# Kernel tuning notes

Measured on AMD Instinct MI355X. Metric: run time of the kernel, lower is better.

The kernel has to match this reference:

```python
import jax, jax.numpy as jnp
import numpy as np

EPS = 1e-5
elu = jax.nn.elu

def bn(x, g, b):
    # BatchNorm (training-mode stats), channel axis = 1
    axes = tuple(i for i in range(x.ndim) if i != 1)
    m = x.mean(axes, keepdims=True)
    v = x.var(axes, keepdims=True)
    shp = [1] * x.ndim; shp[1] = -1
    return g.reshape(shp) * (x - m) * jax.lax.rsqrt(v + EPS) + b.reshape(shp)

def setup_inputs() -> dict:
    key = jax.random.key(0)
    B, N, M, K, C, H, O = 8, 8192, 2048, 16, 128, 64, 256
    ks = jax.random.split(key, 16)
    d = {}
    d['q_points'] = jax.random.normal(ks[0], (B, 3, M), jnp.float32)
    d['s_points'] = jax.random.normal(ks[1], (B, 3, N), jnp.float32)
    d['s_feats'] = jax.random.normal(ks[2], (B, C, N), jnp.float32)
    d['f1_w'] = jax.random.normal(ks[3], (H, 3), jnp.float32) * 0.1
    d['f1_b'] = jnp.zeros((H,), jnp.float32); d['f1_g'] = jnp.ones((H,), jnp.float32); d['f1_be'] = jnp.zeros((H,), jnp.float32)
    d['f2_w'] = jax.random.normal(ks[4], (H, H), jnp.float32) * 0.1
    d['f2_b'] = jnp.zeros((H,), jnp.float32); d['f2_g'] = jnp.ones((H,), jnp.float32); d['f2_be'] = jnp.zeros((H,), jnp.float32)
    d['stem_w'] = jax.random.normal(ks[5], (K * K, 3, K), jnp.float32) * 0.1
    d['stem_b'] = jnp.zeros((K * K,), jnp.float32); d['stem_g'] = jnp.ones((K * K,), jnp.float32); d['stem_be'] = jnp.zeros((K * K,), jnp.float32)
    d['x1_w'] = jax.random.normal(ks[6], (K, K, K), jnp.float32) * 0.1
    d['x1_b'] = jnp.zeros((K * K,), jnp.float32); d['x1_g'] = jnp.ones((K * K,), jnp.float32); d['x1_be'] = jnp.zeros((K * K,), jnp.float32)
    d['x2_w'] = jax.random.normal(ks[7], (K, K, K), jnp.float32) * 0.1
    d['x2_b'] = jnp.zeros((K * K,), jnp.float32); d['x2_g'] = jnp.ones((K * K,), jnp.float32); d['x2_be'] = jnp.zeros((K * K,), jnp.float32)
    d['dw_w'] = jax.random.normal(ks[8], (C + H, K), jnp.float32) * 0.1
    d['pw_w'] = jax.random.normal(ks[9], (O, C + H), jnp.float32) * 0.1
    d['pw_b'] = jnp.zeros((O,), jnp.float32); d['sep_g'] = jnp.ones((O,), jnp.float32); d['sep_be'] = jnp.zeros((O,), jnp.float32)
    d['neighbor_indices'] = jax.random.randint(ks[10], (B, M, K), 0, N, jnp.int64)
    return d

def reference(q_points, s_points, s_feats, f1_w, f1_b, f1_g, f1_be,
              f2_w, f2_b, f2_g, f2_be, stem_w, stem_b, stem_g, stem_be,
              x1_w, x1_b, x1_g, x1_be, x2_w, x2_b, x2_g, x2_be,
              dw_w, pw_w, pw_b, sep_g, sep_be, neighbor_indices):
    B, _, M = q_points.shape
    K = neighbor_indices.shape[2]
    bidx = jnp.arange(B)[:, None, None]
    # group_gather: [B,3,M,K] neighbor coords, centered on queries
    sp = jnp.swapaxes(s_points, 1, 2)                      # [B,N,3]
    aligned = jnp.transpose(sp[bidx, neighbor_indices], (0, 3, 1, 2)) - q_points[:, :, :, None]
    sf = jnp.swapaxes(s_feats, 1, 2)                       # [B,N,C]
    nbr = jnp.transpose(sf[bidx, neighbor_indices], (0, 3, 1, 2))  # [B,C,M,K]
    # f_shared_mlp: two 1x1 conv blocks (conv -> ELU -> BN)
    h = bn(elu(jnp.einsum('bcmk,oc->bomk', aligned, f1_w) + f1_b[None, :, None, None]), f1_g, f1_be)
    h = bn(elu(jnp.einsum('bcmk,oc->bomk', h, f2_w) + f2_b[None, :, None, None]), f2_g, f2_be)
    nf = jnp.concatenate([nbr, h], axis=1)                 # [B,C+H,M,K]
    # X-transform shared MLP: stem Conv2d(3 -> K*K, (1,K))
    t = jnp.einsum('bcmk,ock->bom', aligned, stem_w) + stem_b[None, :, None]
    t = bn(elu(t), stem_g, stem_be).reshape(B, K, K, M)    # [B,g,j,M]
    for w, bb, g, be in ((x1_w, x1_b, x1_g, x1_be), (x2_w, x2_b, x2_g, x2_be)):
        # grouped Conv2d(K -> K*K, (K,1), groups=K)
        y = jnp.einsum('bgjm,gpj->bgpm', t, w) + bb.reshape(1, K, K, 1)
        y = bn(elu(y.reshape(B, K * K, M)), g, be).reshape(B, K, K, M)
        t = jnp.swapaxes(y, 1, 2)                          # XReshape transpose(1,2)
    x = jnp.transpose(t, (0, 3, 2, 1))                     # [B,M,K,K]
    # batched matmul: feats^T @ X
    qf = jnp.einsum('bcmk,bmkl->bcml', nf, x)              # [B,C+H,M,K]
    # SeparableConv2d (1,K): depthwise over K then pointwise 1x1, ELU, BN
    dw = jnp.einsum('bcmk,ck->bcm', qf, dw_w)
    out = jnp.einsum('bcm,oc->bom', dw, pw_w) + pw_b[None, :, None]
    out = bn(elu(out), sep_g, sep_be)                      # [B,O,M]
    return out
```

## Files before the change

### kernel.cpp

```cpp
#include <hip/hip_runtime.h>
#include <hip/hip_bf16.h>
#include <cstddef>
#include <cstdint>

constexpr int cB = 8, cN = 8192, cM = 2048, cK = 16, cC = 128, cH = 64, cO = 256, cCH = 192;
constexpr int NPTS = cB * cM;
constexpr float cEPS = 1e-5f;

typedef __attribute__((ext_vector_type(8))) short short8;
typedef __attribute__((ext_vector_type(4))) float f32x4;

constexpr size_t ACC_BN1 = 0, ACC_BN2 = 128, ACC_STEM = 256, ACC_X1 = 768, ACC_X2 = 1280, ACC_FIN = 1792;
constexpr size_t OFF_SFT = 8192;
constexpr size_t OFF_H1  = OFF_SFT + (size_t)cB * cN * 64;
constexpr size_t OFF_TST = OFF_H1 + (size_t)NPTS * 512;
constexpr size_t OFF_Y1  = OFF_TST + (size_t)NPTS * 128;
constexpr size_t OFF_Y2  = OFF_Y1 + (size_t)NPTS * 256;
constexpr size_t OFF_DW  = OFF_Y1;
constexpr size_t WS_FLOATS = OFF_Y2 + (size_t)NPTS * 256;

__device__ __forceinline__ float eluf(float x) { return x > 0.f ? x : __expf(x) - 1.f; }

__device__ __forceinline__ uint32_t pk2bf(float a, float b) {
    uint32_t ua = __float_as_uint(a); ua += 0x7FFFu + ((ua >> 16) & 1u);
    uint32_t ub = __float_as_uint(b); ub += 0x7FFFu + ((ub >> 16) & 1u);
    return (ua >> 16) | (ub & 0xFFFF0000u);
}
__device__ __forceinline__ float bf_lo(uint32_t u) { return __uint_as_float(u << 16); }
__device__ __forceinline__ float bf_hi(uint32_t u) { return __uint_as_float(u & 0xFFFF0000u); }
__device__ __forceinline__ uint16_t f2bf_u(float a) {
    uint32_t ua = __float_as_uint(a); ua += 0x7FFFu + ((ua >> 16) & 1u);
    return (uint16_t)(ua >> 16);
}

#define WAVE_SYNC() do { asm volatile("s_waitcnt lgkmcnt(0)" ::: "memory"); \
                         __builtin_amdgcn_sched_barrier(0); } while (0)

__global__ __launch_bounds__(256) void k_tr(const float* __restrict__ sf, float* __restrict__ ws) {
    __shared__ float tA[32][33];
    __shared__ float tBt[32][33];
    int b = blockIdx.z, n0 = blockIdx.x * 32, c0 = blockIdx.y * 32;
    int tx = threadIdx.x, ty = threadIdx.y;
    #pragma unroll
    for (int j = 0; j < 32; j += 8) {
        tA[ty + j][tx]  = sf[((size_t)b * cC + (c0 + ty + j)) * cN + n0 + tx];
        tBt[ty + j][tx] = sf[((size_t)b * cC + 64 + (c0 + ty + j)) * cN + n0 + tx];
    }
    __syncthreads();
    uint32_t* out = (uint32_t*)(ws + OFF_SFT);
    #pragma unroll
    for (int j = 0; j < 32; j += 8)
        out[((size_t)b * cN + (n0 + ty + j)) * 64 + c0 + tx] = pk2bf(tA[tx][ty + j], tBt[tx][ty + j]);
}

__global__ __launch_bounds__(256) void kA(const float* __restrict__ qp, const float* __restrict__ sp,
        const float* __restrict__ f1w, const float* __restrict__ f1b,
        const float* __restrict__ stw, const float* __restrict__ stb,
        const int* __restrict__ nidx, float* __restrict__ ws) {
    __shared__ float alw[4][4][48];
    __shared__ __align__(16) uint16_t albs[16][64];
    __shared__ __align__(16) uint16_t bounce[4][16][64];
    __shared__ float red[640];
    int t = threadIdx.x, lane = t & 63, w = t >> 6;
    int ncol = lane & 15, g = lane >> 4;
    for (int l = t; l < 640; l += 256) red[l] = 0.f;
    __syncthreads();
    short8 bfr[4][2];
    float sbias[4];
    #pragma unroll
    for (int tt = 0; tt < 4; tt++) {
        int o = w*64 + tt*16 + ncol;
        sbias[tt] = stb[o];
        #pragma unroll
        for (int s = 0; s < 2; s++) {
            short8 bb;
            #pragma unroll
            for (int j = 0; j < 8; j++) {
                int Kk = s*32 + g*8 + j;
                bb[j] = (Kk < 48) ? (short)f2bf_u(stw[(size_t)o*48 + Kk]) : (short)0;
            }
            bfr[tt][s] = bb;
        }
    }
    float w0 = f1w[lane*3], w1 = f1w[lane*3+1], w2 = f1w[lane*3+2], fb = f1b[lane];
    int pt0 = blockIdx.x * 16;
    {
        int p = lane >> 4, k = lane & 15;
        int row = w*4 + p;
        int pt = pt0 + row, b = pt >> 11, m = pt & (cM - 1);
        int id = nidx[(size_t)pt * cK + k];
        #pragma unroll
        for (int c = 0; c < 3; c++) {
            float v = sp[((size_t)b*3 + c)*cN + id] - qp[((size_t)b*3 + c)*cM + m];
            alw[w][p][c*16 + k] = v;
            int bo = ((c*16 + k)*2) ^ ((row & 7) << 4);
            *(uint16_t*)((char*)&albs[row][0] + bo) = f2bf_u(v);
        }
        int bo = ((48 + k)*2) ^ ((row & 7) << 4);
        *(uint16_t*)((char*)&albs[row][0] + bo) = 0;
    }
    WAVE_SYNC();
    uint4* h1q4 = (uint4*)(ws + OFF_H1);
    float ps1 = 0, pss1 = 0;
    for (int p = 0; p < 4; p++) {
        int pt = pt0 + w*4 + p;
        #pragma unroll
        for (int k = 0; k < 16; k++) {
            float a0 = alw[w][p][k], a1 = alw[w][p][16 + k], a2 = alw[w][p][32 + k];
            float e = eluf(fb + w0*a0 + w1*a1 + w2*a2);
            ps1 += e; pss1 += e*e;
            bounce[w][k][lane] = f2bf_u(e);
        }
        WAVE_SYNC();
        const uint4* src = (const uint4*)&bounce[w][0][0];
        h1q4[(size_t)pt*128 + lane]      = src[lane];
        h1q4[(size_t)pt*128 + 64 + lane] = src[64 + lane];
        WAVE_SYNC();
    }
    atomicAdd(&red[512 + lane], ps1); atomicAdd(&red[576 + lane], pss1);
    __syncthreads();
    uint16_t* tstt = (uint16_t*)&bounce[0][0][0];
    short8 a0, a1;
    {
        int b0 = (g*16) ^ ((ncol & 7) << 4);
        int b1 = (64 + g*16) ^ ((ncol & 7) << 4);
        a0 = *(const short8*)((const char*)&albs[ncol][0] + b0);
        a1 = *(const short8*)((const char*)&albs[ncol][0] + b1);
    }
    #pragma unroll
    for (int tt = 0; tt < 4; tt++) {
        f32x4 acc = {0.f, 0.f, 0.f, 0.f};
        acc = __builtin_amdgcn_mfma_f32_16x16x32_bf16(a0, bfr[tt][0], acc, 0, 0, 0);
        acc = __builtin_amdgcn_mfma_f32_16x16x32_bf16(a1, bfr[tt][1], acc, 0, 0, 0);
        int o = w*64 + tt*16 + ncol;
        float ps2 = 0, pss2 = 0;
        #pragma unroll
        for (int r = 0; r < 4; r++) {
            float e = eluf(acc[r] + sbias[tt]);
            ps2 += e; pss2 += e*e;
            tstt[(g*4 + r)*256 + o] = f2bf_u(e);
        }
        atomicAdd(&red[o], ps2); atomicAdd(&red[256 + o], pss2);
    }
    __syncthreads();
    {
        uint4* tst4 = (uint4*)(ws + OFF_TST);
        const uint4* srcT = (const uint4*)tstt;
        tst4[(size_t)pt0*32 + t]       = srcT[t];
        tst4[(size_t)pt0*32 + 256 + t] = srcT[256 + t];
    }
    atomicAdd(&ws[ACC_STEM + t], red[t]);
    atomicAdd(&ws[ACC_STEM + 256 + t], red[256 + t]);
    if (t < 64) { atomicAdd(&ws[ACC_BN1 + t], red[512 + t]); atomicAdd(&ws[ACC_BN1 + 64 + t], red[576 + t]); }
}

__global__ __launch_bounds__(256) void kE(const float* __restrict__ x1w, const float* __restrict__ x1b,
        const float* __restrict__ stg, const float* __restrict__ stbe, float* __restrict__ ws) {
    __shared__ float xw[256 * 17];
    __shared__ float ts[4][4][256];
    __shared__ float red[512];
    int t = threadIdx.x, lane = t & 63, w = t >> 6;
    for (int l = t; l < 4096; l += 256) xw[(l >> 4)*17 + (l & 15)] = x1w[l];
    for (int l = t; l < 512; l += 256) red[l] = 0.f;
    float sscl[4], sshf[4];
    #pragma unroll
    for (int i = 0; i < 4; i++) {
        int ch = lane*4 + i;
        float mn = ws[ACC_STEM + ch] * (1.f/16384.f);
        float vr = ws[ACC_STEM + 256 + ch] * (1.f/16384.f) - mn*mn;
        float s = stg[ch] * rsqrtf(vr + cEPS);
        sscl[i] = s; sshf[i] = stbe[ch] - mn*s;
    }
    float xb[4];
    #pragma unroll
    for (int q = 0; q < 4; q++) xb[q] = x1b[lane + 64*q];
    __syncthreads();
    const uint16_t* tstb = (const uint16_t*)(ws + OFF_TST);
    int pt0 = blockIdx.x * 16 + w * 4;
    #pragma unroll
    for (int p = 0; p < 4; p++) {
        uint2 v2 = *(const uint2*)&tstb[(size_t)(pt0 + p)*256 + lane*4];
        ts[w][p][lane*4+0] = sscl[0]*bf_lo(v2.x) + sshf[0];
        ts[w][p][lane*4+1] = sscl[1]*bf_hi(v2.x) + sshf[1];
        ts[w][p][lane*4+2] = sscl[2]*bf_lo(v2.y) + sshf[2];
        ts[w][p][lane*4+3] = sscl[3]*bf_hi(v2.y) + sshf[3];
    }
    WAVE_SYNC();
    float ps[4] = {0,0,0,0}, pss[4] = {0,0,0,0};
    #pragma unroll
    for (int q = 0; q < 4; q++) {
        int o = lane + 64*q, g = o >> 4;
        float accp[4] = {xb[q], xb[q], xb[q], xb[q]};
        #pragma unroll
        for (int j4 = 0; j4 < 4; j4++) {
            float s0 = xw[o*17 + j4*4], s1 = xw[o*17 + j4*4+1], s2 = xw[o*17 + j4*4+2], s3 = xw[o*17 + j4*4+3];
            #pragma unroll
            for (int p = 0; p < 4; p++) {
                float4 a = *(const float4*)&ts[w][p][g*16 + j4*4];
                accp[p] += s0*a.x + s1*a.y + s2*a.z + s3*a.w;
            }
        }
        #pragma unroll
        for (int p = 0; p < 4; p++) {
            float e = eluf(accp[p]);
            ps[q] += e; pss[q] += e*e;
            ws[OFF_Y1 + (size_t)(pt0 + p)*256 + o] = e;
        }
    }
    #pragma unroll
    for (int q = 0; q < 4; q++) {
        atomicAdd(&red[lane + 64*q], ps[q]);
        atomicAdd(&red[256 + lane + 64*q], pss[q]);
    }
    __syncthreads();
    atomicAdd(&ws[ACC_X1 + t], red[t]); atomicAdd(&ws[ACC_X1 + 256 + t], red[256 + t]);
}

__global__ __launch_bounds__(256) void kG(const float* __restrict__ x2w, const float* __restrict__ x2b,
        const float* __restrict__ x1g, const float* __restrict__ x1be, float* __restrict__ ws) {
    __shared__ float xw[256 * 17];
    __shared__ float ts[4][4][256];
    __shared__ float red[512];
    int t = threadIdx.x, lane = t & 63, w = t >> 6;
    for (int l = t; l < 4096; l += 256) xw[(l >> 4)*17 + (l & 15)] = x2w[l];
    for (int l = t; l < 512; l += 256) red[l] = 0.f;
    float sscl[4], sshf[4];
    #pragma unroll
    for (int i = 0; i < 4; i++) {
        int ch = lane*4 + i;
        float mn = ws[ACC_X1 + ch] * (1.f/16384.f);
        float vr = ws[ACC_X1 + 256 + ch] * (1.f/16384.f) - mn*mn;
        float s = x1g[ch] * rsqrtf(vr + cEPS);
        sscl[i] = s; sshf[i] = x1be[ch] - mn*s;
    }
    float xb[4];
    #pragma unroll
    for (int q = 0; q < 4; q++) xb[q] = x2b[lane + 64*q];
    __syncthreads();
    int pt0 = blockIdx.x * 16 + w * 4;
    #pragma unroll
    for (int p = 0; p < 4; p++) {
        float4 v = *(const float4*)&ws[OFF_Y1 + (size_t)(pt0 + p)*256 + lane*4];
        float vv[4] = { sscl[0]*v.x + sshf[0], sscl[1]*v.y + sshf[1],
                        sscl[2]*v.z + sshf[2], sscl[3]*v.w + sshf[3] };
        #pragma unroll
        for (int i = 0; i < 4; i++) {
            int ch = lane*4 + i;
            ts[w][p][((ch & 15) << 4) | (ch >> 4)] = vv[i];
        }
    }
    WAVE_SYNC();
    float ps[4] = {0,0,0,0}, pss[4] = {0,0,0,0};
    #pragma unroll
    for (int q = 0; q < 4; q++) {
        int o = lane + 64*q, g = o >> 4;
        float accp[4] = {xb[q], xb[q], xb[q], xb[q]};
        #pragma unroll
        for (int j4 = 0; j4 < 4; j4++) {
            float s0 = xw[o*17 + j4*4], s1 = xw[o*17 + j4*4+1], s2 = xw[o*17 + j4*4+2], s3 = xw[o*17 + j4*4+3];
            #pragma unroll
            for (int p = 0; p < 4; p++) {
                float4 a = *(const float4*)&ts[w][p][g*16 + j4*4];
                accp[p] += s0*a.x + s1*a.y + s2*a.z + s3*a.w;
            }
        }
        #pragma unroll
        for (int p = 0; p < 4; p++) {
            float e = eluf(accp[p]);
            ps[q] += e; pss[q] += e*e;
            ws[OFF_Y2 + (size_t)(pt0 + p)*256 + o] = e;
        }
    }
    #pragma unroll
    for (int q = 0; q < 4; q++) {
        atomicAdd(&red[lane + 64*q], ps[q]);
        atomicAdd(&red[256 + lane + 64*q], pss[q]);
    }
    __syncthreads();
    atomicAdd(&ws[ACC_X2 + t], red[t]); atomicAdd(&ws[ACC_X2 + 256 + t], red[256 + t]);
}

__global__ __launch_bounds__(256) void kC(const float* __restrict__ f2w, const float* __restrict__ f2b,
        const float* __restrict__ f1g, const float* __restrict__ f1be, float* __restrict__ ws) {
    __shared__ float s1s[64], sh1s[64], b2s[64];
    __shared__ float red[128];
    int t = threadIdx.x, lane = t & 63, w = t >> 6;
    if (t < 128) red[t] = 0.f;
    if (t < 64) {
        float mn = ws[ACC_BN1 + t] * (1.f/262144.f);
        float vr = ws[ACC_BN1 + 64 + t] * (1.f/262144.f) - mn*mn;
        float s = f1g[t] * rsqrtf(vr + cEPS);
        s1s[t] = s; sh1s[t] = f1be[t] - mn*s;
    }
    __syncthreads();
    int ncol = lane & 15, g = lane >> 4;
    if (t < 64) {
        float a = f2b[t];
        const float* fr = f2w + (size_t)t*64;
        #pragma unroll 8
        for (int c = 0; c < 64; c++) a += fr[c] * sh1s[c];
        b2s[t] = a;
    }
    short8 bfr[4][2];
    #pragma unroll
    for (int tt = 0; tt < 4; tt++) {
        int o = tt*16 + ncol;
        #pragma unroll
        for (int s = 0; s < 2; s++) {
            short8 bb;
            #pragma unroll
            for (int j = 0; j < 8; j++) {
                int c = s*32 + g*8 + j;
                bb[j] = (short)f2bf_u(f2w[(size_t)o*64 + c] * s1s[c]);
            }
            bfr[tt][s] = bb;
        }
    }
    __syncthreads();
    float bias2[4];
    #pragma unroll
    for (int tt = 0; tt < 4; tt++) bias2[tt] = b2s[tt*16 + ncol];
    const uint4* h1q = (const uint4*)(ws + OFF_H1);
    uint32_t* h2p = (uint32_t*)(ws + OFF_H1);
    int pt0 = blockIdx.x * 16 + w * 4;
    uint4 afrA0 = h1q[(size_t)(pt0+0)*128 + ncol*8 + g];
    uint4 afrA1 = h1q[(size_t)(pt0+0)*128 + ncol*8 + 4 + g];
    uint4 afrB0 = h1q[(size_t)(pt0+1)*128 + ncol*8 + g];
    uint4 afrB1 = h1q[(size_t)(pt0+1)*128 + ncol*8 + 4 + g];
    uint4 afrC0 = h1q[(size_t)(pt0+2)*128 + ncol*8 + g];
    uint4 afrC1 = h1q[(size_t)(pt0+2)*128 + ncol*8 + 4 + g];
    uint4 afrD0 = h1q[(size_t)(pt0+3)*128 + ncol*8 + g];
    uint4 afrD1 = h1q[(size_t)(pt0+3)*128 + ncol*8 + 4 + g];
    float ps[4] = {0,0,0,0}, pss[4] = {0,0,0,0};
    #pragma unroll
    for (int p = 0; p < 4; p++) {
        uint4 a0u = (p == 0) ? afrA0 : (p == 1) ? afrB0 : (p == 2) ? afrC0 : afrD0;
        uint4 a1u = (p == 0) ? afrA1 : (p == 1) ? afrB1 : (p == 2) ? afrC1 : afrD1;
        short8 a0, a1;
        __builtin_memcpy(&a0, &a0u, 16);
        __builtin_memcpy(&a1, &a1u, 16);
        int pt = pt0 + p;
        #pragma unroll
        for (int tt = 0; tt < 4; tt++) {
            f32x4 acc = {0.f, 0.f, 0.f, 0.f};
            acc = __builtin_amdgcn_mfma_f32_16x16x32_bf16(a0, bfr[tt][0], acc, 0, 0, 0);
            acc = __builtin_amdgcn_mfma_f32_16x16x32_bf16(a1, bfr[tt][1], acc, 0, 0, 0);
            float e0 = eluf(acc[0] + bias2[tt]);
            float e1 = eluf(acc[1] + bias2[tt]);
            float e2 = eluf(acc[2] + bias2[tt]);
            float e3 = eluf(acc[3] + bias2[tt]);
            ps[tt]  += e0+e1+e2+e3;
            pss[tt] += e0*e0+e1*e1+e2*e2+e3*e3;
            int o = tt*16 + ncol;
            *(uint2*)(h2p + (size_t)pt*512 + o*8 + g*2) = make_uint2(pk2bf(e0, e1), pk2bf(e2, e3));
        }
    }
    #pragma unroll
    for (int tt = 0; tt < 4; tt++) {
        int o = tt*16 + ncol;
        atomicAdd(&red[o], ps[tt]); atomicAdd(&red[64 + o], pss[tt]);
    }
    __syncthreads();
    if (t < 64) { atomicAdd(&ws[ACC_BN2 + t], red[t]); atomicAdd(&ws[ACC_BN2 + 64 + t], red[64 + t]); }
}

__global__ __launch_bounds__(256) void kI(const float* __restrict__ dww,
        const float* __restrict__ f2g, const float* __restrict__ f2be,
        const float* __restrict__ x2g, const float* __restrict__ x2be,
        const int* __restrict__ nidx, float* __restrict__ ws) {
    __shared__ float dws[192 * 17];
    __shared__ float xs[4][256];
    const uint32_t* h2p = (const uint32_t*)(ws + OFF_H1);
    const uint32_t* sfp = (const uint32_t*)(ws + OFF_SFT);
    int t = threadIdx.x, lane = t & 63, w = t >> 6;
    for (int l = t; l < 3072; l += 256) dws[(l >> 4)*17 + (l & 15)] = dww[l];
    float sx[4], shx[4];
    #pragma unroll
    for (int i = 0; i < 4; i++) {
        int ch = lane*4 + i;
        float mn = ws[ACC_X2 + ch] * (1.f/16384.f);
        float vr = ws[ACC_X2 + 256 + ch] * (1.f/16384.f) - mn*mn;
        float s = x2g[ch] * rsqrtf(vr + cEPS);
        sx[i] = s; shx[i] = x2be[ch] - mn*s;
    }
    float s2, sh2;
    {
        float mn = ws[ACC_BN2 + lane] * (1.f/262144.f);
        float vr = ws[ACC_BN2 + 64 + lane] * (1.f/262144.f) - mn*mn;
        s2 = f2g[lane] * rsqrtf(vr + cEPS);
        sh2 = f2be[lane] - mn*s2;
    }
    __syncthreads();
    uint16_t* dwb = (uint16_t*)(ws + OFF_DW);
    int pt0 = blockIdx.x * 8 + w * 2;
    for (int p = 0; p < 2; p++) {
        int pt = pt0 + p, b = pt >> 11;
        const int4* ip = (const int4*)(nidx + (size_t)pt * cK);
        int4 iA = ip[0], iB = ip[1], iC2 = ip[2], iD = ip[3];
        int idxv[16] = {iA.x, iA.y, iA.z, iA.w, iB.x, iB.y, iB.z, iB.w,
                        iC2.x, iC2.y, iC2.z, iC2.w, iD.x, iD.y, iD.z, iD.w};
        float nfa[16], nfb[16];
        #pragma unroll
        for (int k = 0; k < 16; k++) {
            uint32_t u = sfp[((size_t)b*cN + idxv[k]) * 64 + lane];
            nfa[k] = bf_lo(u); nfb[k] = bf_hi(u);
        }
        float nfh[16];
        {
            const uint4* srcq = (const uint4*)(h2p + (size_t)pt*512 + lane*8);
            uint4 ha = srcq[0], hbq = srcq[1];
            nfh[0]  = s2*bf_lo(ha.x)  + sh2; nfh[1]  = s2*bf_hi(ha.x)  + sh2;
            nfh[2]  = s2*bf_lo(ha.y)  + sh2; nfh[3]  = s2*bf_hi(ha.y)  + sh2;
            nfh[4]  = s2*bf_lo(ha.z)  + sh2; nfh[5]  = s2*bf_hi(ha.z)  + sh2;
            nfh[6]  = s2*bf_lo(ha.w)  + sh2; nfh[7]  = s2*bf_hi(ha.w)  + sh2;
            nfh[8]  = s2*bf_lo(hbq.x) + sh2; nfh[9]  = s2*bf_hi(hbq.x) + sh2;
            nfh[10] = s2*bf_lo(hbq.y) + sh2; nfh[11] = s2*bf_hi(hbq.y) + sh2;
            nfh[12] = s2*bf_lo(hbq.z) + sh2; nfh[13] = s2*bf_hi(hbq.z) + sh2;
            nfh[14] = s2*bf_lo(hbq.w) + sh2; nfh[15] = s2*bf_hi(hbq.w) + sh2;
        }
        {
            float4 v = *(const float4*)&ws[OFF_Y2 + (size_t)pt*256 + lane*4];
            v.x = sx[0]*v.x + shx[0]; v.y = sx[1]*v.y + shx[1];
            v.z = sx[2]*v.z + shx[2]; v.w = sx[3]*v.w + shx[3];
            *(float4*)&xs[w][lane*4] = v;
        }
        WAVE_SYNC();
        float qc[16];
        #pragma unroll
        for (int l = 0; l < 16; l++) qc[l] = 0.f;
        #pragma unroll
        for (int k = 0; k < 16; k++) {
            float4 x0 = *(const float4*)&xs[w][k*16 + 0];
            float4 x1 = *(const float4*)&xs[w][k*16 + 4];
            float4 x2v = *(const float4*)&xs[w][k*16 + 8];
            float4 x3 = *(const float4*)&xs[w][k*16 + 12];
            float nh = nfh[k];
            qc[0] += nh*x0.x; qc[1] += nh*x0.y; qc[2]  += nh*x0.z; qc[3]  += nh*x0.w;
            qc[4] += nh*x1.x; qc[5] += nh*x1.y; qc[6]  += nh*x1.z; qc[7]  += nh*x1.w;
            qc[8] += nh*x2v.x; qc[9] += nh*x2v.y; qc[10] += nh*x2v.z; qc[11] += nh*x2v.w;
            qc[12] += nh*x3.x; qc[13] += nh*x3.y; qc[14] += nh*x3.z; qc[15] += nh*x3.w;
        }
        float dc = 0;
        #pragma unroll
        for (int l = 0; l < 16; l++) dc += qc[l] * dws[(lane + 128)*17 + l];
        float qa[16], qb[16];
        #pragma unroll
        for (int l = 0; l < 16; l++) { qa[l] = 0.f; qb[l] = 0.f; }
        #pragma unroll
        for (int k = 0; k < 16; k++) {
            float4 x0 = *(const float4*)&xs[w][k*16 + 0];
            float4 x1 = *(const float4*)&xs[w][k*16 + 4];
            float4 x2v = *(const float4*)&xs[w][k*16 + 8];
            float4 x3 = *(const float4*)&xs[w][k*16 + 12];
            float na = nfa[k], nb = nfb[k];
            qa[0] += na*x0.x; qa[1] += na*x0.y; qa[2]  += na*x0.z; qa[3]  += na*x0.w;
            qa[4] += na*x1.x; qa[5] += na*x1.y; qa[6]  += na*x1.z; qa[7]  += na*x1.w;
            qa[8] += na*x2v.x; qa[9] += na*x2v.y; qa[10] += na*x2v.z; qa[11] += na*x2v.w;
            qa[12] += na*x3.x; qa[13] += na*x3.y; qa[14] += na*x3.z; qa[15] += na*x3.w;
            qb[0] += nb*x0.x; qb[1] += nb*x0.y; qb[2]  += nb*x0.z; qb[3]  += nb*x0.w;
            qb[4] += nb*x1.x; qb[5] += nb*x1.y; qb[6]  += nb*x1.z; qb[7]  += nb*x1.w;
            qb[8] += nb*x2v.x; qb[9] += nb*x2v.y; qb[10] += nb*x2v.z; qb[11] += nb*x2v.w;
            qb[12] += nb*x3.x; qb[13] += nb*x3.y; qb[14] += nb*x3.z; qb[15] += nb*x3.w;
        }
        float da = 0, db = 0;
        #pragma unroll
        for (int l = 0; l < 16; l++) {
            da += qa[l] * dws[lane*17 + l];
            db += qb[l] * dws[(lane + 64)*17 + l];
        }
        uint16_t* op = dwb + (size_t)pt * cCH;
        op[lane] = f2bf_u(da); op[lane + 64] = f2bf_u(db); op[lane + 128] = f2bf_u(dc);
        WAVE_SYNC();
    }
}

__global__ __launch_bounds__(256) void kJ(const float* __restrict__ pww, const float* __restrict__ pwb,
                                          float* __restrict__ ws, float* __restrict__ out) {
    __shared__ float red[128];
    int t = threadIdx.x, lane = t & 63, w = t >> 6;
    int ncol = lane & 15, g = lane >> 4;
    if (t < 128) red[t] = 0.f;
    __syncthreads();
    int p0 = blockIdx.x * 64;
    int otile = blockIdx.y * 64 + w * 16;
    short8 afr[6];
    #pragma unroll
    for (int kt = 0; kt < 6; kt++) {
        const float* src = pww + (size_t)(otile + ncol) * cCH + kt*32 + g*8;
        float4 v0 = *(const float4*)src;
        float4 v1 = *(const float4*)(src + 4);
        short8 aa;
        aa[0] = (short)f2bf_u(v0.x); aa[1] = (short)f2bf_u(v0.y);
        aa[2] = (short)f2bf_u(v0.z); aa[3] = (short)f2bf_u(v0.w);
        aa[4] = (short)f2bf_u(v1.x); aa[5] = (short)f2bf_u(v1.y);
        aa[6] = (short)f2bf_u(v1.z); aa[7] = (short)f2bf_u(v1.w);
        afr[kt] = aa;
    }
    float pb[4];
    #pragma unroll
    for (int r = 0; r < 4; r++) pb[r] = pwb[otile + g*4 + r];
    const uint16_t* dwb = (const uint16_t*)(ws + OFF_DW);
    int bb = p0 >> 11, mb0 = p0 & (cM - 1);
    float psum[4] = {0,0,0,0}, pssq[4] = {0,0,0,0};
    #pragma unroll
    for (int mt = 0; mt < 4; mt++) {
        const uint16_t* brow = dwb + (size_t)(p0 + mt*16 + ncol) * cCH;
        f32x4 acc = {0.f, 0.f, 0.f, 0.f};
        #pragma unroll
        for (int kt = 0; kt < 6; kt++) {
            short8 bfr = *(const short8*)&brow[kt*32 + g*8];
            acc = __builtin_amdgcn_mfma_f32_16x16x32_bf16(afr[kt], bfr, acc, 0, 0, 0);
        }
        #pragma unroll
        for (int r = 0; r < 4; r++) {
            float e = eluf(acc[r] + pb[r]);
            psum[r] += e; pssq[r] += e*e;
            out[((size_t)bb*cO + otile + g*4 + r)*cM + mb0 + mt*16 + ncol] = e;
        }
    }
    #pragma unroll
    for (int r = 0; r < 4; r++) {
        float s_ = psum[r], q_ = pssq[r];
        #pragma unroll
        for (int off = 1; off < 16; off <<= 1) { s_ += __shfl_xor(s_, off); q_ += __shfl_xor(q_, off); }
        if (ncol == 0) {
            atomicAdd(&red[w*16 + g*4 + r], s_);
            atomicAdd(&red[64 + w*16 + g*4 + r], q_);
        }
    }
    __syncthreads();
    if (t < 64) {
        atomicAdd(&ws[ACC_FIN + blockIdx.y*64 + t], red[t]);
        atomicAdd(&ws[ACC_FIN + 256 + blockIdx.y*64 + t], red[64 + t]);
    }
}

__global__ __launch_bounds__(256) void kK(float* __restrict__ out, const float* __restrict__ ws,
        const float* __restrict__ sepg, const float* __restrict__ sepbe) {
    int i = blockIdx.x * 256 + threadIdx.x;
    if (i < (cB*cO*cM) / 4) {
        int o = (i >> 9) & 255;
        float mn = ws[ACC_FIN + o] * (1.f/16384.f);
        float vr = ws[ACC_FIN + 256 + o] * (1.f/16384.f) - mn*mn;
        float s = sepg[o] * rsqrtf(vr + cEPS);
        float sh = sepbe[o] - mn*s;
        float4 v = ((float4*)out)[i];
        v.x = s*v.x + sh; v.y = s*v.y + sh; v.z = s*v.z + sh; v.w = s*v.w + sh;
        ((float4*)out)[i] = v;
    }
}

extern "C" void kernel_launch(void* const* d_in, const int* in_sizes, int n_in,
                              void* d_out, int out_size, void* d_ws, size_t ws_size,
                              hipStream_t stream) {
    const float* qp   = (const float*)d_in[0];
    const float* sp   = (const float*)d_in[1];
    const float* sf   = (const float*)d_in[2];
    const float* f1w  = (const float*)d_in[3];
    const float* f1b  = (const float*)d_in[4];
    const float* f1g  = (const float*)d_in[5];
    const float* f1be = (const float*)d_in[6];
    const float* f2w  = (const float*)d_in[7];
    const float* f2b  = (const float*)d_in[8];
    const float* f2g  = (const float*)d_in[9];
    const float* f2be = (const float*)d_in[10];
    const float* stw  = (const float*)d_in[11];
    const float* stb  = (const float*)d_in[12];
    const float* stg  = (const float*)d_in[13];
    const float* stbe = (const float*)d_in[14];
    const float* x1w  = (const float*)d_in[15];
    const float* x1b  = (const float*)d_in[16];
    const float* x1g  = (const float*)d_in[17];
    const float* x1be = (const float*)d_in[18];
    const float* x2w  = (const float*)d_in[19];
    const float* x2b  = (const float*)d_in[20];
    const float* x2g  = (const float*)d_in[21];
    const float* x2be = (const float*)d_in[22];
    const float* dww  = (const float*)d_in[23];
    const float* pww  = (const float*)d_in[24];
    const float* pwb  = (const float*)d_in[25];
    const float* sepg = (const float*)d_in[26];
    const float* sepbe= (const float*)d_in[27];
    const int*   nidx = (const int*)d_in[28];
    float* ws  = (float*)d_ws;
    float* out = (float*)d_out;
    if (ws_size < WS_FLOATS * sizeof(float)) return;

    hipMemsetAsync(d_ws, 0, 2304 * sizeof(float), stream);
    k_tr<<<dim3(cN/32, 2, cB), dim3(32, 8), 0, stream>>>(sf, ws);
    kA<<<NPTS/16, 256, 0, stream>>>(qp, sp, f1w, f1b, stw, stb, nidx, ws);
    kE<<<NPTS/16, 256, 0, stream>>>(x1w, x1b, stg, stbe, ws);
    kG<<<NPTS/16, 256, 0, stream>>>(x2w, x2b, x1g, x1be, ws);
    kC<<<NPTS/16, 256, 0, stream>>>(f2w, f2b, f1g, f1be, ws);
    kI<<<NPTS/8,  256, 0, stream>>>(dww, f2g, f2be, x2g, x2be, nidx, ws);
    kJ<<<dim3(NPTS/64, cO/64), 256, 0, stream>>>(pww, pwb, ws, out);
    kK<<<(cB*cO*cM/4 + 255)/256, 256, 0, stream>>>(out, ws, sepg, sepbe);
}
```

Measured before the change: 249.3 us.

## Recompute h1 in kC instead of storing it; store Y1/Y2 as bf16

```diff
diff --git a/kernel.cpp b/kernel.cpp
--- a/kernel.cpp
+++ b/kernel.cpp
@@ -12,8 +12,8 @@
 
 constexpr size_t ACC_BN1 = 0, ACC_BN2 = 128, ACC_STEM = 256, ACC_X1 = 768, ACC_X2 = 1280, ACC_FIN = 1792;
 constexpr size_t OFF_SFT = 8192;
-constexpr size_t OFF_H1  = OFF_SFT + (size_t)cB * cN * 64;
-constexpr size_t OFF_TST = OFF_H1 + (size_t)NPTS * 512;
+constexpr size_t OFF_H2  = OFF_SFT + (size_t)cB * cN * 64;
+constexpr size_t OFF_TST = OFF_H2 + (size_t)NPTS * 512;
 constexpr size_t OFF_Y1  = OFF_TST + (size_t)NPTS * 128;
 constexpr size_t OFF_Y2  = OFF_Y1 + (size_t)NPTS * 256;
 constexpr size_t OFF_DW  = OFF_Y1;
@@ -59,7 +59,7 @@
         const int* __restrict__ nidx, float* __restrict__ ws) {
     __shared__ float alw[4][4][48];
     __shared__ __align__(16) uint16_t albs[16][64];
-    __shared__ __align__(16) uint16_t bounce[4][16][64];
+    __shared__ __align__(16) uint16_t tstt[16][256];
     __shared__ float red[640];
     int t = threadIdx.x, lane = t & 63, w = t >> 6;
     int ncol = lane & 15, g = lane >> 4;
@@ -100,26 +100,18 @@
         *(uint16_t*)((char*)&albs[row][0] + bo) = 0;
     }
     WAVE_SYNC();
-    uint4* h1q4 = (uint4*)(ws + OFF_H1);
     float ps1 = 0, pss1 = 0;
+    #pragma unroll
     for (int p = 0; p < 4; p++) {
-        int pt = pt0 + w*4 + p;
         #pragma unroll
         for (int k = 0; k < 16; k++) {
             float a0 = alw[w][p][k], a1 = alw[w][p][16 + k], a2 = alw[w][p][32 + k];
             float e = eluf(fb + w0*a0 + w1*a1 + w2*a2);
             ps1 += e; pss1 += e*e;
-            bounce[w][k][lane] = f2bf_u(e);
-        }
-        WAVE_SYNC();
-        const uint4* src = (const uint4*)&bounce[w][0][0];
-        h1q4[(size_t)pt*128 + lane]      = src[lane];
-        h1q4[(size_t)pt*128 + 64 + lane] = src[64 + lane];
-        WAVE_SYNC();
+        }
     }
     atomicAdd(&red[512 + lane], ps1); atomicAdd(&red[576 + lane], pss1);
     __syncthreads();
-    uint16_t* tstt = (uint16_t*)&bounce[0][0][0];
     short8 a0, a1;
     {
         int b0 = (g*16) ^ ((ncol & 7) << 4);
@@ -138,20 +130,117 @@
         for (int r = 0; r < 4; r++) {
             float e = eluf(acc[r] + sbias[tt]);
             ps2 += e; pss2 += e*e;
-            tstt[(g*4 + r)*256 + o] = f2bf_u(e);
+            tstt[g*4 + r][o] = f2bf_u(e);
         }
         atomicAdd(&red[o], ps2); atomicAdd(&red[256 + o], pss2);
     }
     __syncthreads();
     {
         uint4* tst4 = (uint4*)(ws + OFF_TST);
-        const uint4* srcT = (const uint4*)tstt;
+        const uint4* srcT = (const uint4*)&tstt[0][0];
         tst4[(size_t)pt0*32 + t]       = srcT[t];
         tst4[(size_t)pt0*32 + 256 + t] = srcT[256 + t];
     }
     atomicAdd(&ws[ACC_STEM + t], red[t]);
     atomicAdd(&ws[ACC_STEM + 256 + t], red[256 + t]);
     if (t < 64) { atomicAdd(&ws[ACC_BN1 + t], red[512 + t]); atomicAdd(&ws[ACC_BN1 + 64 + t], red[576 + t]); }
+}
+
+__global__ __launch_bounds__(256) void kC(const float* __restrict__ qp, const float* __restrict__ sp,
+        const float* __restrict__ f1w, const float* __restrict__ f1b,
+        const float* __restrict__ f2w, const float* __restrict__ f2b,
+        const float* __restrict__ f1g, const float* __restrict__ f1be,
+        const int* __restrict__ nidx, float* __restrict__ ws) {
+    __shared__ float al4[4][48];
+    __shared__ __align__(16) unsigned char h1l[4][2048];
+    __shared__ float s1s[64], sh1s[64], b2s[64];
+    __shared__ float red[128];
+    uint32_t* h2p = (uint32_t*)(ws + OFF_H2);
+    int t = threadIdx.x, lane = t & 63, w = t >> 6;
+    if (t < 128) red[t] = 0.f;
+    if (t < 64) {
+        float mn = ws[ACC_BN1 + t] * (1.f/262144.f);
+        float vr = ws[ACC_BN1 + 64 + t] * (1.f/262144.f) - mn*mn;
+        float s = f1g[t] * rsqrtf(vr + cEPS);
+        s1s[t] = s; sh1s[t] = f1be[t] - mn*s;
+    }
+    __syncthreads();
+    float w0 = f1w[lane*3], w1 = f1w[lane*3+1], w2 = f1w[lane*3+2], fb = f1b[lane];
+    int ncol = lane & 15, g = lane >> 4;
+    if (t < 64) {
+        float a = f2b[t];
+        const float* fr = f2w + (size_t)t*64;
+        #pragma unroll 8
+        for (int c = 0; c < 64; c++) a += fr[c] * sh1s[c];
+        b2s[t] = a;
+    }
+    short8 bfr[4][2];
+    #pragma unroll
+    for (int tt = 0; tt < 4; tt++) {
+        int o = tt*16 + ncol;
+        #pragma unroll
+        for (int s = 0; s < 2; s++) {
+            short8 bb;
+            #pragma unroll
+            for (int j = 0; j < 8; j++) {
+                int c = s*32 + g*8 + j;
+                bb[j] = (short)f2bf_u(f2w[(size_t)o*64 + c] * s1s[c]);
+            }
+            bfr[tt][s] = bb;
+        }
+    }
+    __syncthreads();
+    float bias2[4];
+    #pragma unroll
+    for (int tt = 0; tt < 4; tt++) bias2[tt] = b2s[tt*16 + ncol];
+    float ps[4] = {0,0,0,0}, pss[4] = {0,0,0,0};
+    int pt0 = blockIdx.x * 16 + w * 4;
+    for (int p = 0; p < 4; p++) {
+        int pt = pt0 + p, b = pt >> 11, m = pt & (cM - 1);
+        if (lane < 48) {
+            int c = lane >> 4, k = lane & 15;
+            int id = nidx[(size_t)pt * cK + k];
+            al4[w][c*16 + k] = sp[((size_t)b*3 + c)*cN + id] - qp[((size_t)b*3 + c)*cM + m];
+        }
+        WAVE_SYNC();
+        #pragma unroll
+        for (int k = 0; k < 16; k++) {
+            float a0 = al4[w][k], a1 = al4[w][16 + k], a2 = al4[w][32 + k];
+            float e = eluf(fb + w0*a0 + w1*a1 + w2*a2);
+            int byteoff = (lane*2) ^ ((k & 7) << 4);
+            *(uint16_t*)&h1l[w][k*128 + byteoff] = (uint16_t)f2bf_u(e);
+        }
+        WAVE_SYNC();
+        short8 a0v, a1v;
+        {
+            int b0 = (g*16) ^ ((ncol & 7) << 4);
+            int b1 = (64 + g*16) ^ ((ncol & 7) << 4);
+            a0v = *(const short8*)&h1l[w][ncol*128 + b0];
+            a1v = *(const short8*)&h1l[w][ncol*128 + b1];
+        }
+        WAVE_SYNC();
+        #pragma unroll
+        for (int tt = 0; tt < 4; tt++) {
+            f32x4 acc = {0.f, 0.f, 0.f, 0.f};
+            acc = __builtin_amdgcn_mfma_f32_16x16x32_bf16(a0v, bfr[tt][0], acc, 0, 0, 0);
+            acc = __builtin_amdgcn_mfma_f32_16x16x32_bf16(a1v, bfr[tt][1], acc, 0, 0, 0);
+            float e0 = eluf(acc[0] + bias2[tt]);
+            float e1 = eluf(acc[1] + bias2[tt]);
+            float e2 = eluf(acc[2] + bias2[tt]);
+            float e3 = eluf(acc[3] + bias2[tt]);
+            ps[tt]  += e0+e1+e2+e3;
+            pss[tt] += e0*e0+e1*e1+e2*e2+e3*e3;
+            int o = tt*16 + ncol;
+            *(uint2*)(h2p + (size_t)pt*512 + o*8 + g*2) = make_uint2(pk2bf(e0, e1), pk2bf(e2, e3));
+        }
+    }
+    #pragma unroll
+    for (int tt = 0; tt < 4; tt++) {
+        int o = tt*16 + ncol;
+        atomicAdd(&red[o], ps[tt]); atomicAdd(&red[64 + o], pss[tt]);
+    }
+    __syncthreads();
+    if (t < 64) { atomicAdd(&ws[ACC_BN2 + t], red[t]); atomicAdd(&ws[ACC_BN2 + 64 + t], red[64 + t]); }
 }
 
 __global__ __launch_bounds__(256) void kE(const float* __restrict__ x1w, const float* __restrict__ x1b,
@@ -171,9 +260,6 @@
         float s = stg[ch] * rsqrtf(vr + cEPS);
         sscl[i] = s; sshf[i] = stbe[ch] - mn*s;
     }
-    float xb[4];
-    #pragma unroll
-    for (int q = 0; q < 4; q++) xb[q] = x1b[lane + 64*q];
     __syncthreads();
     const uint16_t* tstb = (const uint16_t*)(ws + OFF_TST);
     int pt0 = blockIdx.x * 16 + w * 4;
@@ -186,31 +272,35 @@
         ts[w][p][lane*4+3] = sscl[3]*bf_hi(v2.y) + sshf[3];
     }
     WAVE_SYNC();
-    float ps[4] = {0,0,0,0}, pss[4] = {0,0,0,0};
-    #pragma unroll
-    for (int q = 0; q < 4; q++) {
-        int o = lane + 64*q, g = o >> 4;
-        float accp[4] = {xb[q], xb[q], xb[q], xb[q]};
+    float eo[4][4];
+    #pragma unroll
+    for (int sl = 0; sl < 4; sl++) {
+        int o = (sl < 2) ? (lane*2 + sl) : (128 + lane*2 + sl - 2);
+        int gg = o >> 4;
+        float bia = x1b[o];
+        float a0 = bia, a1 = bia, a2 = bia, a3 = bia;
         #pragma unroll
         for (int j4 = 0; j4 < 4; j4++) {
             float s0 = xw[o*17 + j4*4], s1 = xw[o*17 + j4*4+1], s2 = xw[o*17 + j4*4+2], s3 = xw[o*17 + j4*4+3];
-            #pragma unroll
-            for (int p = 0; p < 4; p++) {
-                float4 a = *(const float4*)&ts[w][p][g*16 + j4*4];
-                accp[p] += s0*a.x + s1*a.y + s2*a.z + s3*a.w;
-            }
-        }
-        #pragma unroll
-        for (int p = 0; p < 4; p++) {
-            float e = eluf(accp[p]);
-            ps[q] += e; pss[q] += e*e;
-            ws[OFF_Y1 + (size_t)(pt0 + p)*256 + o] = e;
-        }
-    }
-    #pragma unroll
-    for (int q = 0; q < 4; q++) {
-        atomicAdd(&red[lane + 64*q], ps[q]);
-        atomicAdd(&red[256 + lane + 64*q], pss[q]);
+            float4 t0 = *(const float4*)&ts[w][0][gg*16 + j4*4];
+            float4 t1 = *(const float4*)&ts[w][1][gg*16 + j4*4];
+            float4 t2 = *(const float4*)&ts[w][2][gg*16 + j4*4];
+            float4 t3 = *(const float4*)&ts[w][3][gg*16 + j4*4];
+            a0 += s0*t0.x + s1*t0.y + s2*t0.z + s3*t0.w;
+            a1 += s0*t1.x + s1*t1.y + s2*t1.z + s3*t1.w;
+            a2 += s0*t2.x + s1*t2.y + s2*t2.z + s3*t2.w;
+            a3 += s0*t3.x + s1*t3.y + s2*t3.z + s3*t3.w;
+        }
+        eo[0][sl] = eluf(a0); eo[1][sl] = eluf(a1); eo[2][sl] = eluf(a2); eo[3][sl] = eluf(a3);
+        float ps = eo[0][sl]+eo[1][sl]+eo[2][sl]+eo[3][sl];
+        float qs = eo[0][sl]*eo[0][sl]+eo[1][sl]*eo[1][sl]+eo[2][sl]*eo[2][sl]+eo[3][sl]*eo[3][sl];
+        atomicAdd(&red[o], ps); atomicAdd(&red[256 + o], qs);
+    }
+    uint32_t* y1p = (uint32_t*)(ws + OFF_Y1);
+    #pragma unroll
+    for (int p = 0; p < 4; p++) {
+        y1p[(size_t)(pt0 + p)*128 + lane]      = pk2bf(eo[p][0], eo[p][1]);
+        y1p[(size_t)(pt0 + p)*128 + 64 + lane] = pk2bf(eo[p][2], eo[p][3]);
     }
     __syncthreads();
     atomicAdd(&ws[ACC_X1 + t], red[t]); atomicAdd(&ws[ACC_X1 + 256 + t], red[256 + t]);
@@ -233,16 +323,14 @@
         float s = x1g[ch] * rsqrtf(vr + cEPS);
         sscl[i] = s; sshf[i] = x1be[ch] - mn*s;
     }
-    float xb[4];
-    #pragma unroll
-    for (int q = 0; q < 4; q++) xb[q] = x2b[lane + 64*q];
-    __syncthreads();
+    __syncthreads();
+    const uint32_t* y1p = (const uint32_t*)(ws + OFF_Y1);
     int pt0 = blockIdx.x * 16 + w * 4;
     #pragma unroll
     for (int p = 0; p < 4; p++) {
-        float4 v = *(const float4*)&ws[OFF_Y1 + (size_t)(pt0 + p)*256 + lane*4];
-        float vv[4] = { sscl[0]*v.x + sshf[0], sscl[1]*v.y + sshf[1],
-                        sscl[2]*v.z + sshf[2], sscl[3]*v.w + sshf[3] };
+        uint2 v2 = *(const uint2*)(y1p + (size_t)(pt0 + p)*128 + lane*2);
+        float vv[4] = { sscl[0]*bf_lo(v2.x) + sshf[0], sscl[1]*bf_hi(v2.x) + sshf[1],
+                        sscl[2]*bf_lo(v2.y) + sshf[2], sscl[3]*bf_hi(v2.y) + sshf[3] };
         #pragma unroll
         for (int i = 0; i < 4; i++) {
             int ch = lane*4 + i;
@@ -250,118 +338,38 @@
         }
     }
     WAVE_SYNC();
-    float ps[4] = {0,0,0,0}, pss[4] = {0,0,0,0};
-    #pragma unroll
-    for (int q = 0; q < 4; q++) {
-        int o = lane + 64*q, g = o >> 4;
-        float accp[4] = {xb[q], xb[q], xb[q], xb[q]};
+    float eo[4][4];
+    #pragma unroll
+    for (int sl = 0; sl < 4; sl++) {
+        int o = (sl < 2) ? (lane*2 + sl) : (128 + lane*2 + sl - 2);
+        int gg = o >> 4;
+        float bia = x2b[o];
+        float a0 = bia, a1 = bia, a2 = bia, a3 = bia;
         #pragma unroll
         for (int j4 = 0; j4 < 4; j4++) {
             float s0 = xw[o*17 + j4*4], s1 = xw[o*17 + j4*4+1], s2 = xw[o*17 + j4*4+2], s3 = xw[o*17 + j4*4+3];
-            #pragma unroll
-            for (int p = 0; p < 4; p++) {
-                float4 a = *(const float4*)&ts[w][p][g*16 + j4*4];
-                accp[p] += s0*a.x + s1*a.y + s2*a.z + s3*a.w;
-            }
-        }
-        #pragma unroll
-        for (int p = 0; p < 4; p++) {
-            float e = eluf(accp[p]);
-            ps[q] += e; pss[q] += e*e;
-            ws[OFF_Y2 + (size_t)(pt0 + p)*256 + o] = e;
-        }
-    }
-    #pragma unroll
-    for (int q = 0; q < 4; q++) {
-        atomicAdd(&red[lane + 64*q], ps[q]);
-        atomicAdd(&red[256 + lane + 64*q], pss[q]);
+            float4 t0 = *(const float4*)&ts[w][0][gg*16 + j4*4];
+            float4 t1 = *(const float4*)&ts[w][1][gg*16 + j4*4];
+            float4 t2 = *(const float4*)&ts[w][2][gg*16 + j4*4];
+            float4 t3 = *(const float4*)&ts[w][3][gg*16 + j4*4];
+            a0 += s0*t0.x + s1*t0.y + s2*t0.z + s3*t0.w;
+            a1 += s0*t1.x + s1*t1.y + s2*t1.z + s3*t1.w;
+            a2 += s0*t2.x + s1*t2.y + s2*t2.z + s3*t2.w;
+            a3 += s0*t3.x + s1*t3.y + s2*t3.z + s3*t3.w;
+        }
+        eo[0][sl] = eluf(a0); eo[1][sl] = eluf(a1); eo[2][sl] = eluf(a2); eo[3][sl] = eluf(a3);
+        float ps = eo[0][sl]+eo[1][sl]+eo[2][sl]+eo[3][sl];
+        float qs = eo[0][sl]*eo[0][sl]+eo[1][sl]*eo[1][sl]+eo[2][sl]*eo[2][sl]+eo[3][sl]*eo[3][sl];
+        atomicAdd(&red[o], ps); atomicAdd(&red[256 + o], qs);
+    }
+    uint32_t* y2p = (uint32_t*)(ws + OFF_Y2);
+    #pragma unroll
+    for (int p = 0; p < 4; p++) {
+        y2p[(size_t)(pt0 + p)*128 + lane]      = pk2bf(eo[p][0], eo[p][1]);
+        y2p[(size_t)(pt0 + p)*128 + 64 + lane] = pk2bf(eo[p][2], eo[p][3]);
     }
     __syncthreads();
     atomicAdd(&ws[ACC_X2 + t], red[t]); atomicAdd(&ws[ACC_X2 + 256 + t], red[256 + t]);
-}
-
-__global__ __launch_bounds__(256) void kC(const float* __restrict__ f2w, const float* __restrict__ f2b,
-        const float* __restrict__ f1g, const float* __restrict__ f1be, float* __restrict__ ws) {
-    __shared__ float s1s[64], sh1s[64], b2s[64];
-    __shared__ float red[128];
-    int t = threadIdx.x, lane = t & 63, w = t >> 6;
-    if (t < 128) red[t] = 0.f;
-    if (t < 64) {
-        float mn = ws[ACC_BN1 + t] * (1.f/262144.f);
-        float vr = ws[ACC_BN1 + 64 + t] * (1.f/262144.f) - mn*mn;
-        float s = f1g[t] * rsqrtf(vr + cEPS);
-        s1s[t] = s; sh1s[t] = f1be[t] - mn*s;
-    }
-    __syncthreads();
-    int ncol = lane & 15, g = lane >> 4;
-    if (t < 64) {
-        float a = f2b[t];
-        const float* fr = f2w + (size_t)t*64;
-        #pragma unroll 8
-        for (int c = 0; c < 64; c++) a += fr[c] * sh1s[c];
-        b2s[t] = a;
-    }
-    short8 bfr[4][2];
-    #pragma unroll
-    for (int tt = 0; tt < 4; tt++) {
-        int o = tt*16 + ncol;
-        #pragma unroll
-        for (int s = 0; s < 2; s++) {
-            short8 bb;
-            #pragma unroll
-            for (int j = 0; j < 8; j++) {
-                int c = s*32 + g*8 + j;
-                bb[j] = (short)f2bf_u(f2w[(size_t)o*64 + c] * s1s[c]);
-            }
-            bfr[tt][s] = bb;
-        }
-    }
-    __syncthreads();
-    float bias2[4];
-    #pragma unroll
-    for (int tt = 0; tt < 4; tt++) bias2[tt] = b2s[tt*16 + ncol];
-    const uint4* h1q = (const uint4*)(ws + OFF_H1);
-    uint32_t* h2p = (uint32_t*)(ws + OFF_H1);
-    int pt0 = blockIdx.x * 16 + w * 4;
-    uint4 afrA0 = h1q[(size_t)(pt0+0)*128 + ncol*8 + g];
-    uint4 afrA1 = h1q[(size_t)(pt0+0)*128 + ncol*8 + 4 + g];
-    uint4 afrB0 = h1q[(size_t)(pt0+1)*128 + ncol*8 + g];
-    uint4 afrB1 = h1q[(size_t)(pt0+1)*128 + ncol*8 + 4 + g];
-    uint4 afrC0 = h1q[(size_t)(pt0+2)*128 + ncol*8 + g];
-    uint4 afrC1 = h1q[(size_t)(pt0+2)*128 + ncol*8 + 4 + g];
-    uint4 afrD0 = h1q[(size_t)(pt0+3)*128 + ncol*8 + g];
-    uint4 afrD1 = h1q[(size_t)(pt0+3)*128 + ncol*8 + 4 + g];
-    float ps[4] = {0,0,0,0}, pss[4] = {0,0,0,0};
-    #pragma unroll
-    for (int p = 0; p < 4; p++) {
-        uint4 a0u = (p == 0) ? afrA0 : (p == 1) ? afrB0 : (p == 2) ? afrC0 : afrD0;
-        uint4 a1u = (p == 0) ? afrA1 : (p == 1) ? afrB1 : (p == 2) ? afrC1 : afrD1;
-        short8 a0, a1;
-        __builtin_memcpy(&a0, &a0u, 16);
-        __builtin_memcpy(&a1, &a1u, 16);
-        int pt = pt0 + p;
-        #pragma unroll
-        for (int tt = 0; tt < 4; tt++) {
-            f32x4 acc = {0.f, 0.f, 0.f, 0.f};
-            acc = __builtin_amdgcn_mfma_f32_16x16x32_bf16(a0, bfr[tt][0], acc, 0, 0, 0);
-            acc = __builtin_amdgcn_mfma_f32_16x16x32_bf16(a1, bfr[tt][1], acc, 0, 0, 0);
-            float e0 = eluf(acc[0] + bias2[tt]);
-            float e1 = eluf(acc[1] + bias2[tt]);
-            float e2 = eluf(acc[2] + bias2[tt]);
-            float e3 = eluf(acc[3] + bias2[tt]);
-            ps[tt]  += e0+e1+e2+e3;
-            pss[tt] += e0*e0+e1*e1+e2*e2+e3*e3;
-            int o = tt*16 + ncol;
-            *(uint2*)(h2p + (size_t)pt*512 + o*8 + g*2) = make_uint2(pk2bf(e0, e1), pk2bf(e2, e3));
-        }
-    }
-    #pragma unroll
-    for (int tt = 0; tt < 4; tt++) {
-        int o = tt*16 + ncol;
-        atomicAdd(&red[o], ps[tt]); atomicAdd(&red[64 + o], pss[tt]);
-    }
-    __syncthreads();
-    if (t < 64) { atomicAdd(&ws[ACC_BN2 + t], red[t]); atomicAdd(&ws[ACC_BN2 + 64 + t], red[64 + t]); }
 }
 
 __global__ __launch_bounds__(256) void kI(const float* __restrict__ dww,
@@ -370,8 +378,9 @@
         const int* __restrict__ nidx, float* __restrict__ ws) {
     __shared__ float dws[192 * 17];
     __shared__ float xs[4][256];
-    const uint32_t* h2p = (const uint32_t*)(ws + OFF_H1);
+    const uint32_t* h2p = (const uint32_t*)(ws + OFF_H2);
     const uint32_t* sfp = (const uint32_t*)(ws + OFF_SFT);
+    const uint32_t* y2p = (const uint32_t*)(ws + OFF_Y2);
     int t = threadIdx.x, lane = t & 63, w = t >> 6;
     for (int l = t; l < 3072; l += 256) dws[(l >> 4)*17 + (l & 15)] = dww[l];
     float sx[4], shx[4];
@@ -419,10 +428,11 @@
             nfh[14] = s2*bf_lo(hbq.w) + sh2; nfh[15] = s2*bf_hi(hbq.w) + sh2;
         }
         {
-            float4 v = *(const float4*)&ws[OFF_Y2 + (size_t)pt*256 + lane*4];
-            v.x = sx[0]*v.x + shx[0]; v.y = sx[1]*v.y + shx[1];
-            v.z = sx[2]*v.z + shx[2]; v.w = sx[3]*v.w + shx[3];
-            *(float4*)&xs[w][lane*4] = v;
+            uint2 v2 = *(const uint2*)(y2p + (size_t)pt*128 + lane*2);
+            xs[w][lane*4+0] = sx[0]*bf_lo(v2.x) + shx[0];
+            xs[w][lane*4+1] = sx[1]*bf_hi(v2.x) + shx[1];
+            xs[w][lane*4+2] = sx[2]*bf_lo(v2.y) + shx[2];
+            xs[w][lane*4+3] = sx[3]*bf_hi(v2.y) + shx[3];
         }
         WAVE_SYNC();
         float qc[16];
@@ -589,9 +599,9 @@
     hipMemsetAsync(d_ws, 0, 2304 * sizeof(float), stream);
     k_tr<<<dim3(cN/32, 2, cB), dim3(32, 8), 0, stream>>>(sf, ws);
     kA<<<NPTS/16, 256, 0, stream>>>(qp, sp, f1w, f1b, stw, stb, nidx, ws);
+    kC<<<NPTS/16, 256, 0, stream>>>(qp, sp, f1w, f1b, f2w, f2b, f1g, f1be, nidx, ws);
     kE<<<NPTS/16, 256, 0, stream>>>(x1w, x1b, stg, stbe, ws);
     kG<<<NPTS/16, 256, 0, stream>>>(x2w, x2b, x1g, x1be, ws);
-    kC<<<NPTS/16, 256, 0, stream>>>(f2w, f2b, f1g, f1be, ws);
     kI<<<NPTS/8,  256, 0, stream>>>(dww, f2g, f2be, x2g, x2be, nidx, ws);
     kJ<<<dim3(NPTS/64, cO/64), 256, 0, stream>>>(pww, pwb, ws, out);
     kK<<<(cB*cO*cM/4 + 255)/256, 256, 0, stream>>>(out, ws, sepg, sepbe);
```

Result: no change. 244.6 us (-1.9%).
